# Performance work log

Hardware: AMD Instinct MI355X
Metric: run time of the kernel (lower is better)

The kernel has to match this reference:

```python
import jax, jax.numpy as jnp
import numpy as np

U = 8          # units per modular layer
B = 16384      # batch
IN = 512       # input feature dim
H = 512        # modular hidden dim
NC = 62        # n_class


def _aggregate(P, h):
    # P: [T, F] policy link matrix; h: [F, B, D] per-unit features.
    # agg[t] = sum_f P[t,f] * h[f], normalized by row-sum when row-sum > 0.
    s = jnp.einsum('tf,fbd->tbd', P, h)
    row = P.sum(axis=1)                      # [T]
    safe = jnp.where(row > 0, row, 1.0)[:, None, None]
    return jnp.where((row > 0)[:, None, None], s / safe, s)


def setup_inputs() -> dict:
    key = jax.random.key(0)
    ks = jax.random.split(key, 12)
    s_in = 1.0 / np.sqrt(IN)
    s_h = 1.0 / np.sqrt(H)
    return {
        'x': jax.random.normal(ks[0], (B, IN), jnp.float32),
        'policy1': jax.random.uniform(ks[1], (U * U,), jnp.float32),
        'policy2': jax.random.uniform(ks[2], (U * U,), jnp.float32),
        'policy_final': jax.random.uniform(ks[3], (U,), jnp.float32),
        'W0': jax.random.uniform(ks[4], (U, IN, H), jnp.float32, -s_in, s_in),
        'b0': jax.random.uniform(ks[5], (U, H), jnp.float32, -s_in, s_in),
        'W1': jax.random.uniform(ks[6], (U, H, H), jnp.float32, -s_h, s_h),
        'b1': jax.random.uniform(ks[7], (U, H), jnp.float32, -s_h, s_h),
        'W2': jax.random.uniform(ks[8], (U, H, NC), jnp.float32, -s_h, s_h),
        'b2': jax.random.uniform(ks[9], (U, NC), jnp.float32, -s_h, s_h),
    }


def reference(x, policy1, policy2, policy_final, W0, b0, W1, b1, W2, b2):
    # Layer 0 (input modular layer): policy_list[0] is forced to all-ones,
    # so every unit sees x unscaled. Each unit: Linear + ReLU.
    h0 = jax.nn.relu(jnp.einsum('bi,uid->ubd', x, W0) + b0[:, None, :])  # [U,B,H]

    # Mid layer: policy-gated weighted-sum aggregation, then per-unit Linear+ReLU.
    a1 = _aggregate(policy1.reshape(U, U), h0)
    h1 = jax.nn.relu(jnp.einsum('ubi,uid->ubd', a1, W1) + b1[:, None, :])

    # Output modular layer: aggregate then per-unit Linear (no activation).
    a2 = _aggregate(policy2.reshape(U, U), h1)
    h2 = jnp.einsum('ubi,uic->ubc', a2, W2) + b2[:, None, :]  # [U,B,NC]

    # Final gating. Original code divides by divider INSIDE the unit loop
    # (every iteration), so replicate that recurrence exactly.
    d = policy_final.sum()
    inv = jnp.where(d > 0, 1.0 / jnp.where(d > 0, d, 1.0), 1.0)
    out = jnp.zeros((B, NC), jnp.float32)
    for j in range(U):  # fixed small unit count, not a data dim
        out = (out + h2[j] * policy_final[j]) * inv
    return out
```

## Files before the change

kernel.cpp:

```cpp
#include <hip/hip_runtime.h>

#define U_   8
#define B_   16384
#define NC_  62

typedef __attribute__((ext_vector_type(8))) short bfrag;
typedef __attribute__((ext_vector_type(4))) float facc;

__device__ __forceinline__ float bf2f(unsigned int lo16) {
    union { unsigned int i; float f; } v;
    v.i = lo16 << 16;
    return v.f;
}
__device__ __forceinline__ unsigned short f2bf(float f) {
    unsigned int x = __float_as_uint(f);
    return (unsigned short)((x + 0x7fffu + ((x >> 16) & 1u)) >> 16);
}
__device__ __forceinline__ void gl2lds16(const void* g, void* l) {
    __builtin_amdgcn_global_load_lds(
        (const __attribute__((address_space(1))) void*)g,
        (__attribute__((address_space(3))) void*)l, 16, 0, 0);
}

__global__ void prep_kernel(const float* __restrict__ p1, const float* __restrict__ p2,
                            const float* __restrict__ pf, const float* __restrict__ b2,
                            float* __restrict__ P1n, float* __restrict__ P2n,
                            float* __restrict__ wfin, float* __restrict__ cconst)
{
    int t = threadIdx.x;
    if (t >= 64) return;
    int row = t >> 3;
    float s1 = 0.f, s2 = 0.f;
    for (int f = 0; f < 8; f++) { s1 += p1[row * 8 + f]; s2 += p2[row * 8 + f]; }
    P1n[t] = p1[t] * (s1 > 0.f ? 1.f / s1 : 1.f);
    P2n[t] = p2[t] * (s2 > 0.f ? 1.f / s2 : 1.f);
    float d = 0.f;
    for (int j = 0; j < 8; j++) d += pf[j];
    float inv = d > 0.f ? 1.f / d : 1.f;
    float wv[8];
    for (int j = 0; j < 8; j++) {
        float v = pf[j];
        for (int i = j; i < 8; i++) v *= inv;
        wv[j] = v;
    }
    if (t < 8) wfin[t] = wv[t];
    float cc = 0.f;
    if (t < NC_) for (int u = 0; u < 8; u++) cc += wv[u] * b2[u * NC_ + t];
    cconst[t] = cc;
}

__global__ __launch_bounds__(256) void reorder_w0(
    const float* __restrict__ W0, unsigned short* __restrict__ W0r)
{
    __shared__ float tile[32][33];
    const int u  = blockIdx.z;
    const int n0 = blockIdx.x * 32, k0 = blockIdx.y * 32;
    const int tx = threadIdx.x & 31, ty = threadIdx.x >> 5;
    const float* Wb = W0 + (long)u * 512 * 512;
#pragma unroll
    for (int i = 0; i < 4; i++)
        tile[ty + i * 8][tx] = Wb[(long)(k0 + ty + i * 8) * 512 + n0 + tx];
    __syncthreads();
#pragma unroll
    for (int i = 0; i < 4; i++) {
        int n = n0 + ty + i * 8, k = k0 + tx;
        int np = (n >> 5) * 256 + u * 32 + (n & 31);
        W0r[(long)np * 512 + k] = f2bf(tile[tx][ty + i * 8]);
    }
}

__global__ __launch_bounds__(256) void transpose_w(
    const float* __restrict__ W, unsigned short* __restrict__ Wt)
{
    __shared__ float tile[32][33];
    const int u  = blockIdx.z;
    const int n0 = blockIdx.x * 32, k0 = blockIdx.y * 32;
    const int tx = threadIdx.x & 31, ty = threadIdx.x >> 5;
    const float* Wb = W + (long)u * 512 * 512;
#pragma unroll
    for (int i = 0; i < 4; i++)
        tile[ty + i * 8][tx] = Wb[(long)(k0 + ty + i * 8) * 512 + n0 + tx];
    __syncthreads();
    unsigned short* Wo = Wt + (long)u * 512 * 512;
#pragma unroll
    for (int i = 0; i < 4; i++) {
        int n = n0 + ty + i * 8, k = k0 + tx;
        Wo[(long)n * 512 + k] = f2bf(tile[tx][ty + i * 8]);
    }
}

__global__ __launch_bounds__(256) void wout_build(
    const float* __restrict__ W2, const float* __restrict__ P2n,
    const float* __restrict__ wfin, unsigned short* __restrict__ Woutt)
{
    const int c   = threadIdx.x & 63;
    const int row = blockIdx.x * 4 + (threadIdx.x >> 6);
    const int f = row >> 9, k = row & 511;
    float s = 0.f;
    if (c < NC_) {
#pragma unroll
        for (int u = 0; u < 8; u++)
            s += wfin[u] * P2n[u * 8 + f] * W2[((long)u * 512 + k) * NC_ + c];
    }
    Woutt[(long)c * 4096 + row] = f2bf(s);
}

__global__ __launch_bounds__(256) void convert_x(
    const float* __restrict__ x, unsigned short* __restrict__ xb, long n)
{
    long i = ((long)blockIdx.x * 256 + threadIdx.x) * 8;
    if (i >= n) return;
    const float4* xp = (const float4*)(x + i);
    float4 a = xp[0], b = xp[1];
    uint4 o;
    o.x = f2bf(a.x) | ((unsigned)f2bf(a.y) << 16);
    o.y = f2bf(a.z) | ((unsigned)f2bf(a.w) << 16);
    o.z = f2bf(b.x) | ((unsigned)f2bf(b.y) << 16);
    o.w = f2bf(b.z) | ((unsigned)f2bf(b.w) << 16);
    *(uint4*)(xb + i) = o;
}

__global__ __launch_bounds__(512, 4) void gemm0_mix(
    const unsigned short* __restrict__ xb, const unsigned short* __restrict__ W0r,
    const float* __restrict__ b0, const float* __restrict__ P1n,
    unsigned short* __restrict__ a1, long plane)
{
    __shared__ __align__(16) unsigned short sm[128 * 264];
    unsigned short* sA = sm;
    unsigned short* sB = sm + 128 * 64;
    const int tid = threadIdx.x, w = tid >> 6, lane = tid & 63;
    const int flat = blockIdx.x;
    const int xcd = flat & 7, seq = flat >> 3;
    const int ng = xcd * 2 + (seq & 1);
    const long mBase = (long)(seq >> 1) * 128;

    const int lr = lane >> 3;
    const int lg = (lane & 7) ^ lr;
    const int wm = w >> 2, wn = w & 3;
    const int r = lane & 15, q = lane >> 4;
    const int x7 = r & 7;

    facc acc[4][4];
#pragma unroll
    for (int i = 0; i < 4; i++)
#pragma unroll
        for (int j = 0; j < 4; j++) acc[i][j] = (facc){0.f, 0.f, 0.f, 0.f};

    for (int k0 = 0; k0 < 512; k0 += 64) {
        __syncthreads();
#pragma unroll
        for (int i = 0; i < 2; i++) {
            const int c = w + i * 8;
            gl2lds16(xb + (mBase + c * 8 + lr) * 512 + k0 + lg * 8, sA + c * 512);
        }
#pragma unroll
        for (int i = 0; i < 4; i++) {
            const int c = w * 4 + i;
            gl2lds16(W0r + ((long)ng * 256 + c * 8 + lr) * 512 + k0 + lg * 8,
                     sB + c * 512);
        }
        __syncthreads();
#pragma unroll
        for (int h = 0; h < 2; h++) {
            const int xg = ((h * 4 + q) ^ x7) * 8;
            bfrag aF[4], bF[4];
#pragma unroll
            for (int mt = 0; mt < 4; mt++)
                aF[mt] = *(const bfrag*)&sA[(wm * 64 + mt * 16 + r) * 64 + xg];
#pragma unroll
            for (int nt = 0; nt < 4; nt++)
                bF[nt] = *(const bfrag*)&sB[(wn * 64 + nt * 16 + r) * 64 + xg];
#pragma unroll
            for (int mt = 0; mt < 4; mt++)
#pragma unroll
                for (int nt = 0; nt < 4; nt++)
                    acc[mt][nt] = __builtin_amdgcn_mfma_f32_16x16x32_bf16(
                        aF[mt], bF[nt], acc[mt][nt], 0, 0, 0);
        }
    }

    __syncthreads();
#pragma unroll
    for (int nt = 0; nt < 4; nt++) {
        const int cl = wn * 64 + nt * 16 + r;
        const float bv = b0[(cl >> 5) * 512 + ng * 32 + (cl & 31)];
#pragma unroll
        for (int mt = 0; mt < 4; mt++) {
            const int rowb = wm * 64 + mt * 16 + q * 4;
#pragma unroll
            for (int rg = 0; rg < 4; rg++) {
                float v = acc[mt][nt][rg] + bv;
                v = v > 0.f ? v : 0.f;
                sm[(rowb + rg) * 264 + cl] = f2bf(v);
            }
        }
    }
    __syncthreads();

    float pw[64];
#pragma unroll
    for (int i = 0; i < 64; i++) pw[i] = P1n[i];
    const int row = tid >> 2, fs = (tid & 3) * 8;
    float hv[8][8];
#pragma unroll
    for (int u = 0; u < 8; u++) {
        bfrag hx = *(const bfrag*)&sm[row * 264 + u * 32 + fs];
#pragma unroll
        for (int j = 0; j < 8; j++)
            hv[u][j] = bf2f((unsigned int)(unsigned short)hx[j]);
    }
    const long rowOff = (mBase + row) * 512 + ng * 32 + fs;
#pragma unroll
    for (int t = 0; t < 8; t++) {
        float o[8];
#pragma unroll
        for (int j = 0; j < 8; j++) {
            float s = 0.f;
#pragma unroll
            for (int u = 0; u < 8; u++) s = fmaf(pw[t * 8 + u], hv[u][j], s);
            o[j] = s;
        }
        uint4 ov;
        ov.x = f2bf(o[0]) | ((unsigned)f2bf(o[1]) << 16);
        ov.y = f2bf(o[2]) | ((unsigned)f2bf(o[3]) << 16);
        ov.z = f2bf(o[4]) | ((unsigned)f2bf(o[5]) << 16);
        ov.w = f2bf(o[6]) | ((unsigned)f2bf(o[7]) << 16);
        *(uint4*)(a1 + (long)t * plane + rowOff) = ov;
    }
}

__global__ __launch_bounds__(256, 4) void gemm_h(
    const unsigned short* __restrict__ a1,
    const unsigned short* __restrict__ W1t,
    const float* __restrict__ b1,
    unsigned short* __restrict__ h1, long plane)
{
    __shared__ __align__(16) unsigned short sm[128 * 136];
    unsigned short* sA = sm;
    unsigned short* sB = sm + 128 * 64;
    const int tid = threadIdx.x, w = tid >> 6, lane = tid & 63;
    const int flat = blockIdx.x;
    const int u = flat & 7, seq = flat >> 3;
    const int nBase = (seq & 3) * 128;
    const long mBase = (long)(seq >> 2) * 128;

    const int lr = lane >> 3, lg = (lane & 7) ^ lr;
    const int wm = w >> 1, wn = w & 1;
    const int r = lane & 15, q = lane >> 4;
    const int x7 = r & 7;

    const unsigned short* Ab = a1 + (long)u * plane;
    const unsigned short* Bb = W1t + ((long)u * 512 + nBase) * 512;

    facc acc[4][4];
#pragma unroll
    for (int i = 0; i < 4; i++)
#pragma unroll
        for (int j = 0; j < 4; j++) acc[i][j] = (facc){0.f, 0.f, 0.f, 0.f};

    for (int k0 = 0; k0 < 512; k0 += 64) {
        __syncthreads();
#pragma unroll
        for (int i = 0; i < 4; i++) {
            const int c = w * 4 + i;
            gl2lds16(Ab + (mBase + c * 8 + lr) * 512 + k0 + lg * 8, sA + c * 512);
            gl2lds16(Bb + (long)(c * 8 + lr) * 512 + k0 + lg * 8, sB + c * 512);
        }
        __syncthreads();
#pragma unroll
        for (int h = 0; h < 2; h++) {
            const int xg = ((h * 4 + q) ^ x7) * 8;
            bfrag aF[4], bF[4];
#pragma unroll
            for (int mt = 0; mt < 4; mt++)
                aF[mt] = *(const bfrag*)&sA[(wm * 64 + mt * 16 + r) * 64 + xg];
#pragma unroll
            for (int nt = 0; nt < 4; nt++)
                bF[nt] = *(const bfrag*)&sB[(wn * 64 + nt * 16 + r) * 64 + xg];
#pragma unroll
            for (int mt = 0; mt < 4; mt++)
#pragma unroll
                for (int nt = 0; nt < 4; nt++)
                    acc[mt][nt] = __builtin_amdgcn_mfma_f32_16x16x32_bf16(
                        aF[mt], bF[nt], acc[mt][nt], 0, 0, 0);
        }
    }

    __syncthreads();
#pragma unroll
    for (int nt = 0; nt < 4; nt++) {
        const int col = wn * 64 + nt * 16 + r;
        const float bv = b1[u * 512 + nBase + col];
#pragma unroll
        for (int mt = 0; mt < 4; mt++) {
            const int rowb = wm * 64 + mt * 16 + q * 4;
#pragma unroll
            for (int rg = 0; rg < 4; rg++) {
                float v = acc[mt][nt][rg] + bv;
                v = v > 0.f ? v : 0.f;
                sm[(rowb + rg) * 136 + col] = f2bf(v);
            }
        }
    }
    __syncthreads();

    unsigned short* Cb = h1 + (long)u * plane + mBase * 512 + nBase;
#pragma unroll
    for (int it = 0; it < 8; it++) {
        const int g = tid + it * 256;
        const int row = g >> 4, gr = g & 15;
        *(uint4*)(Cb + (long)row * 512 + gr * 8) = *(const uint4*)&sm[row * 136 + gr * 8];
    }
}

__global__ __launch_bounds__(256, 4) void gemm_out(
    const unsigned short* __restrict__ h1,
    const unsigned short* __restrict__ Bt,
    float* __restrict__ partial, long plane, int Bc)
{
    __shared__ __align__(16) unsigned short sA[64 * 64];
    __shared__ __align__(16) unsigned short sB[64 * 64];
    const int tid = threadIdx.x, w = tid >> 6, lane = tid & 63;
    const int flat = blockIdx.x;
    const int kc = flat & 1;
    const long mBase = (long)(flat >> 1) * 64;

    const int lr = lane >> 3, lg = (lane & 7) ^ lr;
    const int wm = w >> 1, wn = w & 1;
    const int r = lane & 15, q = lane >> 4;
    const int x7 = r & 7;

    facc acc[2][2];
#pragma unroll
    for (int i = 0; i < 2; i++)
#pragma unroll
        for (int j = 0; j < 2; j++) acc[i][j] = (facc){0.f, 0.f, 0.f, 0.f};

    for (int it = 0; it < 32; it++) {
        const int u = kc * 4 + (it >> 3);
        const int kk = (it & 7) * 64;
        __syncthreads();
#pragma unroll
        for (int i = 0; i < 2; i++) {
            const int c = w * 2 + i;
            gl2lds16(h1 + (long)u * plane + (mBase + c * 8 + lr) * 512 + kk + lg * 8,
                     sA + c * 512);
            gl2lds16(Bt + (long)(c * 8 + lr) * 4096 + u * 512 + kk + lg * 8,
                     sB + c * 512);
        }
        __syncthreads();
#pragma unroll
        for (int h = 0; h < 2; h++) {
            const int xg = ((h * 4 + q) ^ x7) * 8;
            bfrag aF[2], bF[2];
#pragma unroll
            for (int mt = 0; mt < 2; mt++)
                aF[mt] = *(const bfrag*)&sA[(wm * 32 + mt * 16 + r) * 64 + xg];
#pragma unroll
            for (int nt = 0; nt < 2; nt++)
                bF[nt] = *(const bfrag*)&sB[(wn * 32 + nt * 16 + r) * 64 + xg];
#pragma unroll
            for (int mt = 0; mt < 2; mt++)
#pragma unroll
                for (int nt = 0; nt < 2; nt++)
                    acc[mt][nt] = __builtin_amdgcn_mfma_f32_16x16x32_bf16(
                        aF[mt], bF[nt], acc[mt][nt], 0, 0, 0);
        }
    }

    float* pb = partial + ((long)kc * Bc + mBase) * 64;
#pragma unroll
    for (int nt = 0; nt < 2; nt++) {
        const int col = wn * 32 + nt * 16 + r;
#pragma unroll
        for (int mt = 0; mt < 2; mt++) {
#pragma unroll
            for (int rg = 0; rg < 4; rg++) {
                const int row = wm * 32 + mt * 16 + q * 4 + rg;
                pb[(long)row * 64 + col] = acc[mt][nt][rg];
            }
        }
    }
}

__global__ __launch_bounds__(256) void reduce_out(
    const float* __restrict__ partial, const float* __restrict__ cconst,
    float* __restrict__ out, int Bc)
{
    const long flat = (long)blockIdx.x * 256 + threadIdx.x;
    const long row = flat >> 2;
    const int cg = (int)(flat & 3) * 16;
    float s[16];
#pragma unroll
    for (int j = 0; j < 16; j++) s[j] = 0.f;
#pragma unroll
    for (int kc = 0; kc < 2; kc++) {
        const float4* p = (const float4*)(partial + ((long)kc * Bc + row) * 64 + cg);
#pragma unroll
        for (int v4 = 0; v4 < 4; v4++) {
            float4 v = p[v4];
            s[v4 * 4 + 0] += v.x; s[v4 * 4 + 1] += v.y;
            s[v4 * 4 + 2] += v.z; s[v4 * 4 + 3] += v.w;
        }
    }
#pragma unroll
    for (int j = 0; j < 16; j++) {
        const int c = cg + j;
        if (c < NC_) out[row * NC_ + c] = s[j] + cconst[c];
    }
}

extern "C" void kernel_launch(void* const* d_in, const int* in_sizes, int n_in,
                              void* d_out, int out_size, void* d_ws, size_t ws_size,
                              hipStream_t stream)
{
    const float* x  = (const float*)d_in[0];
    const float* p1 = (const float*)d_in[1];
    const float* p2 = (const float*)d_in[2];
    const float* pf = (const float*)d_in[3];
    const float* W0 = (const float*)d_in[4];
    const float* b0 = (const float*)d_in[5];
    const float* W1 = (const float*)d_in[6];
    const float* b1 = (const float*)d_in[7];
    const float* W2 = (const float*)d_in[8];
    const float* b2 = (const float*)d_in[9];
    float* out = (float*)d_out;

    char* ws = (char*)d_ws;
    size_t off = 0;
    auto alloc = [&](size_t bytes) -> void* {
        void* p = ws + off;
        off += (bytes + 255) & ~(size_t)255;
        return p;
    };
    float* P1n    = (float*)alloc(64 * sizeof(float));
    float* P2n    = (float*)alloc(64 * sizeof(float));
    float* wfin   = (float*)alloc(8 * sizeof(float));
    float* cconst = (float*)alloc(64 * sizeof(float));
    unsigned short* W0r   = (unsigned short*)alloc((size_t)4096 * 512 * 2);
    unsigned short* W1t   = (unsigned short*)alloc((size_t)U_ * 512 * 512 * 2);
    unsigned short* Woutt = (unsigned short*)alloc((size_t)64 * 4096 * 2);
    unsigned short* xb    = (unsigned short*)alloc((size_t)B_ * 512 * 2);

    size_t remain = ws_size > off ? ws_size - off : 0;
    int Bc = 2048;
    for (int cand = B_; cand >= 2048; cand >>= 1) {
        size_t need = 2ull * 8 * cand * 512 * 2 + 2ull * cand * 64 * 4 + 1024;
        if (need <= remain) { Bc = cand; break; }
    }
    unsigned short* a1 = (unsigned short*)alloc(8ull * Bc * 512 * 2);
    unsigned short* h1 = (unsigned short*)alloc(8ull * Bc * 512 * 2);
    float* partial     = (float*)alloc(2ull * Bc * 64 * 4);

    prep_kernel<<<1, 64, 0, stream>>>(p1, p2, pf, b2, P1n, P2n, wfin, cconst);
    reorder_w0<<<dim3(16, 16, 8), 256, 0, stream>>>(W0, W0r);
    transpose_w<<<dim3(16, 16, 8), 256, 0, stream>>>(W1, W1t);
    wout_build<<<dim3(1024), 256, 0, stream>>>(W2, P2n, wfin, Woutt);
    convert_x<<<dim3(B_ * 512 / 8 / 256), 256, 0, stream>>>(x, xb, (long)B_ * 512);

    const int Mb = Bc / 128;
    const long plane = (long)Bc * 512;
    for (int bb = 0; bb < B_; bb += Bc) {
        gemm0_mix<<<dim3(16 * Mb), 512, 0, stream>>>(
            xb + (long)bb * 512, W0r, b0, P1n, a1, plane);
        gemm_h<<<dim3(32 * Mb), 256, 0, stream>>>(a1, W1t, b1, h1, plane);
        gemm_out<<<dim3(2 * (Bc / 64)), 256, 0, stream>>>(h1, Woutt, partial, plane, Bc);
        reduce_out<<<dim3(Bc / 64), 256, 0, stream>>>(
            partial, cconst, out + (long)bb * NC_, Bc);
    }
}
```

Before: 327.1 us.

## Fuse hidden-layer GEMM with output GEMM to avoid h1 round trip

Merges gemm_h and gemm_out into one kernel. Each block computes a 64-row tile of h1 for two units, one 128-column slab at a time, and stages that slab in LDS as bf16. It then multiplies the slab straight into the output accumulator using Woutt fragments loaded from global memory. This drops the h1 workspace write and read and one launch, at the cost of smaller M tiles (less reuse of W1), more synchronisation, unstaged global loads of B fragments for the second GEMM, and a 4-way partial reduction instead of 2-way.

```diff
diff --git a/kernel.cpp b/kernel.cpp
--- a/kernel.cpp
+++ b/kernel.cpp
@@ -229,146 +229,126 @@
     }
 }
 
-__global__ __launch_bounds__(256, 4) void gemm_h(
+__global__ __launch_bounds__(256, 4) void gemm_h_out(
     const unsigned short* __restrict__ a1,
     const unsigned short* __restrict__ W1t,
     const float* __restrict__ b1,
-    unsigned short* __restrict__ h1, long plane)
-{
-    __shared__ __align__(16) unsigned short sm[128 * 136];
-    unsigned short* sA = sm;
-    unsigned short* sB = sm + 128 * 64;
+    const unsigned short* __restrict__ Woutt,
+    float* __restrict__ partial, long plane, int Bc)
+{
+    __shared__ __align__(16) unsigned short sA[64 * 64];
+    __shared__ __align__(16) unsigned short sB[128 * 64];
+    __shared__ __align__(16) unsigned short sH[2 * 64 * 64];
     const int tid = threadIdx.x, w = tid >> 6, lane = tid & 63;
     const int flat = blockIdx.x;
-    const int u = flat & 7, seq = flat >> 3;
-    const int nBase = (seq & 3) * 128;
-    const long mBase = (long)(seq >> 2) * 128;
+    const int xcd = flat & 7, seq = flat >> 3;
+    const int up = xcd >> 1;
+    const int Mt2 = Bc >> 7;
+    const long mBase = ((long)(xcd & 1) * Mt2 + seq) * 64;
 
     const int lr = lane >> 3, lg = (lane & 7) ^ lr;
     const int wm = w >> 1, wn = w & 1;
     const int r = lane & 15, q = lane >> 4;
     const int x7 = r & 7;
 
-    const unsigned short* Ab = a1 + (long)u * plane;
-    const unsigned short* Bb = W1t + ((long)u * 512 + nBase) * 512;
-
-    facc acc[4][4];
-#pragma unroll
-    for (int i = 0; i < 4; i++)
-#pragma unroll
-        for (int j = 0; j < 4; j++) acc[i][j] = (facc){0.f, 0.f, 0.f, 0.f};
-
-    for (int k0 = 0; k0 < 512; k0 += 64) {
-        __syncthreads();
-#pragma unroll
-        for (int i = 0; i < 4; i++) {
-            const int c = w * 4 + i;
-            gl2lds16(Ab + (mBase + c * 8 + lr) * 512 + k0 + lg * 8, sA + c * 512);
-            gl2lds16(Bb + (long)(c * 8 + lr) * 512 + k0 + lg * 8, sB + c * 512);
-        }
-        __syncthreads();
-#pragma unroll
-        for (int h = 0; h < 2; h++) {
-            const int xg = ((h * 4 + q) ^ x7) * 8;
-            bfrag aF[4], bF[4];
-#pragma unroll
-            for (int mt = 0; mt < 4; mt++)
-                aF[mt] = *(const bfrag*)&sA[(wm * 64 + mt * 16 + r) * 64 + xg];
-#pragma unroll
-            for (int nt = 0; nt < 4; nt++)
-                bF[nt] = *(const bfrag*)&sB[(wn * 64 + nt * 16 + r) * 64 + xg];
-#pragma unroll
-            for (int mt = 0; mt < 4; mt++)
-#pragma unroll
-                for (int nt = 0; nt < 4; nt++)
-                    acc[mt][nt] = __builtin_amdgcn_mfma_f32_16x16x32_bf16(
-                        aF[mt], bF[nt], acc[mt][nt], 0, 0, 0);
-        }
-    }
-
-    __syncthreads();
-#pragma unroll
-    for (int nt = 0; nt < 4; nt++) {
-        const int col = wn * 64 + nt * 16 + r;
-        const float bv = b1[u * 512 + nBase + col];
-#pragma unroll
-        for (int mt = 0; mt < 4; mt++) {
-            const int rowb = wm * 64 + mt * 16 + q * 4;
-#pragma unroll
-            for (int rg = 0; rg < 4; rg++) {
-                float v = acc[mt][nt][rg] + bv;
-                v = v > 0.f ? v : 0.f;
-                sm[(rowb + rg) * 136 + col] = f2bf(v);
+    facc acc2[2][2];
+#pragma unroll
+    for (int i = 0; i < 2; i++)
+#pragma unroll
+        for (int j = 0; j < 2; j++) acc2[i][j] = (facc){0.f, 0.f, 0.f, 0.f};
+
+    for (int iu = 0; iu < 2; iu++) {
+        const int u = up * 2 + iu;
+        const unsigned short* Ab = a1 + (long)u * plane;
+        for (int nb = 0; nb < 4; nb++) {
+            const int nBase = nb * 128;
+            facc acc1[2][4];
+#pragma unroll
+            for (int i = 0; i < 2; i++)
+#pragma unroll
+                for (int j = 0; j < 4; j++) acc1[i][j] = (facc){0.f, 0.f, 0.f, 0.f};
+
+            for (int k0 = 0; k0 < 512; k0 += 64) {
+                __syncthreads();
+#pragma unroll
+                for (int i = 0; i < 2; i++) {
+                    const int c = w * 2 + i;
+                    gl2lds16(Ab + (mBase + c * 8 + lr) * 512 + k0 + lg * 8,
+                             sA + c * 512);
+                }
+#pragma unroll
+                for (int i = 0; i < 4; i++) {
+                    const int c = w * 4 + i;
+                    gl2lds16(W1t + ((long)u * 512 + nBase + c * 8 + lr) * 512
+                                 + k0 + lg * 8, sB + c * 512);
+                }
+                __syncthreads();
+#pragma unroll
+                for (int h = 0; h < 2; h++) {
+                    const int xg = ((h * 4 + q) ^ x7) * 8;
+                    bfrag aF[2], bF[4];
+#pragma unroll
+                    for (int mt = 0; mt < 2; mt++)
+                        aF[mt] = *(const bfrag*)&sA[(wm * 32 + mt * 16 + r) * 64 + xg];
+#pragma unroll
+                    for (int nt = 0; nt < 4; nt++)
+                        bF[nt] = *(const bfrag*)&sB[(wn * 64 + nt * 16 + r) * 64 + xg];
+#pragma unroll
+                    for (int mt = 0; mt < 2; mt++)
+#pragma unroll
+                        for (int nt = 0; nt < 4; nt++)
+                            acc1[mt][nt] = __builtin_amdgcn_mfma_f32_16x16x32_bf16(
+                                aF[mt], bF[nt], acc1[mt][nt], 0, 0, 0);
+                }
             }
-        }
-    }
-    __syncthreads();
-
-    unsigned short* Cb = h1 + (long)u * plane + mBase * 512 + nBase;
-#pragma unroll
-    for (int it = 0; it < 8; it++) {
-        const int g = tid + it * 256;
-        const int row = g >> 4, gr = g & 15;
-        *(uint4*)(Cb + (long)row * 512 + gr * 8) = *(const uint4*)&sm[row * 136 + gr * 8];
-    }
-}
-
-__global__ __launch_bounds__(256, 4) void gemm_out(
-    const unsigned short* __restrict__ h1,
-    const unsigned short* __restrict__ Bt,
-    float* __restrict__ partial, long plane, int Bc)
-{
-    __shared__ __align__(16) unsigned short sA[64 * 64];
-    __shared__ __align__(16) unsigned short sB[64 * 64];
-    const int tid = threadIdx.x, w = tid >> 6, lane = tid & 63;
-    const int flat = blockIdx.x;
-    const int kc = flat & 1;
-    const long mBase = (long)(flat >> 1) * 64;
-
-    const int lr = lane >> 3, lg = (lane & 7) ^ lr;
-    const int wm = w >> 1, wn = w & 1;
-    const int r = lane & 15, q = lane >> 4;
-    const int x7 = r & 7;
-
-    facc acc[2][2];
-#pragma unroll
-    for (int i = 0; i < 2; i++)
-#pragma unroll
-        for (int j = 0; j < 2; j++) acc[i][j] = (facc){0.f, 0.f, 0.f, 0.f};
-
-    for (int it = 0; it < 32; it++) {
-        const int u = kc * 4 + (it >> 3);
-        const int kk = (it & 7) * 64;
-        __syncthreads();
-#pragma unroll
-        for (int i = 0; i < 2; i++) {
-            const int c = w * 2 + i;
-            gl2lds16(h1 + (long)u * plane + (mBase + c * 8 + lr) * 512 + kk + lg * 8,
-                     sA + c * 512);
-            gl2lds16(Bt + (long)(c * 8 + lr) * 4096 + u * 512 + kk + lg * 8,
-                     sB + c * 512);
-        }
-        __syncthreads();
-#pragma unroll
-        for (int h = 0; h < 2; h++) {
-            const int xg = ((h * 4 + q) ^ x7) * 8;
-            bfrag aF[2], bF[2];
-#pragma unroll
-            for (int mt = 0; mt < 2; mt++)
-                aF[mt] = *(const bfrag*)&sA[(wm * 32 + mt * 16 + r) * 64 + xg];
-#pragma unroll
-            for (int nt = 0; nt < 2; nt++)
-                bF[nt] = *(const bfrag*)&sB[(wn * 32 + nt * 16 + r) * 64 + xg];
-#pragma unroll
-            for (int mt = 0; mt < 2; mt++)
-#pragma unroll
-                for (int nt = 0; nt < 2; nt++)
-                    acc[mt][nt] = __builtin_amdgcn_mfma_f32_16x16x32_bf16(
-                        aF[mt], bF[nt], acc[mt][nt], 0, 0, 0);
-        }
-    }
-
-    float* pb = partial + ((long)kc * Bc + mBase) * 64;
+
+#pragma unroll
+            for (int nt = 0; nt < 4; nt++) {
+                const int col = wn * 64 + nt * 16 + r;
+                const float bv = b1[u * 512 + nBase + col];
+                const int slab = col >> 6, cg = (col >> 3) & 7, ce = col & 7;
+#pragma unroll
+                for (int mt = 0; mt < 2; mt++) {
+                    const int rowb = wm * 32 + mt * 16 + q * 4;
+#pragma unroll
+                    for (int rg = 0; rg < 4; rg++) {
+                        const int row = rowb + rg;
+                        float v = acc1[mt][nt][rg] + bv;
+                        v = v > 0.f ? v : 0.f;
+                        sH[slab * 4096 + row * 64 + ((cg ^ (row & 7)) * 8) + ce] = f2bf(v);
+                    }
+                }
+            }
+            __syncthreads();
+
+#pragma unroll
+            for (int ks = 0; ks < 4; ks++) {
+                const int kh = ks >> 1, h2 = ks & 1;
+                bfrag aF2[2], bF2[2];
+#pragma unroll
+                for (int mt = 0; mt < 2; mt++) {
+                    const int row = wm * 32 + mt * 16 + r;
+                    aF2[mt] = *(const bfrag*)&sH[kh * 4096 + row * 64
+                                                 + (((h2 * 4 + q) ^ x7) * 8)];
+                }
+#pragma unroll
+                for (int nt = 0; nt < 2; nt++) {
+                    const int c = wn * 32 + nt * 16 + r;
+                    bF2[nt] = *(const bfrag*)(Woutt + (long)c * 4096 + u * 512
+                                              + nBase + ks * 32 + q * 8);
+                }
+#pragma unroll
+                for (int mt = 0; mt < 2; mt++)
+#pragma unroll
+                    for (int nt = 0; nt < 2; nt++)
+                        acc2[mt][nt] = __builtin_amdgcn_mfma_f32_16x16x32_bf16(
+                            aF2[mt], bF2[nt], acc2[mt][nt], 0, 0, 0);
+            }
+            __syncthreads();
+        }
+    }
+
+    float* pb = partial + ((long)up * Bc + mBase) * 64;
 #pragma unroll
     for (int nt = 0; nt < 2; nt++) {
         const int col = wn * 32 + nt * 16 + r;
@@ -377,7 +357,7 @@
 #pragma unroll
             for (int rg = 0; rg < 4; rg++) {
                 const int row = wm * 32 + mt * 16 + q * 4 + rg;
-                pb[(long)row * 64 + col] = acc[mt][nt][rg];
+                pb[(long)row * 64 + col] = acc2[mt][nt][rg];
             }
         }
     }
@@ -394,8 +374,8 @@
 #pragma unroll
     for (int j = 0; j < 16; j++) s[j] = 0.f;
 #pragma unroll
-    for (int kc = 0; kc < 2; kc++) {
-        const float4* p = (const float4*)(partial + ((long)kc * Bc + row) * 64 + cg);
+    for (int up = 0; up < 4; up++) {
+        const float4* p = (const float4*)(partial + ((long)up * Bc + row) * 64 + cg);
 #pragma unroll
         for (int v4 = 0; v4 < 4; v4++) {
             float4 v = p[v4];
@@ -445,12 +425,11 @@
     size_t remain = ws_size > off ? ws_size - off : 0;
     int Bc = 2048;
     for (int cand = B_; cand >= 2048; cand >>= 1) {
-        size_t need = 2ull * 8 * cand * 512 * 2 + 2ull * cand * 64 * 4 + 1024;
+        size_t need = 8ull * cand * 512 * 2 + 4ull * cand * 64 * 4 + 1024;
         if (need <= remain) { Bc = cand; break; }
     }
     unsigned short* a1 = (unsigned short*)alloc(8ull * Bc * 512 * 2);
-    unsigned short* h1 = (unsigned short*)alloc(8ull * Bc * 512 * 2);
-    float* partial     = (float*)alloc(2ull * Bc * 64 * 4);
+    float* partial     = (float*)alloc(4ull * Bc * 64 * 4);
 
     prep_kernel<<<1, 64, 0, stream>>>(p1, p2, pf, b2, P1n, P2n, wfin, cconst);
     reorder_w0<<<dim3(16, 16, 8), 256, 0, stream>>>(W0, W0r);
@@ -463,8 +442,8 @@
     for (int bb = 0; bb < B_; bb += Bc) {
         gemm0_mix<<<dim3(16 * Mb), 512, 0, stream>>>(
             xb + (long)bb * 512, W0r, b0, P1n, a1, plane);
-        gemm_h<<<dim3(32 * Mb), 256, 0, stream>>>(a1, W1t, b1, h1, plane);
-        gemm_out<<<dim3(2 * (Bc / 64)), 256, 0, stream>>>(h1, Woutt, partial, plane, Bc);
+        gemm_h_out<<<dim3(Bc / 16), 256, 0, stream>>>(
+            a1, W1t, b1, Woutt, partial, plane, Bc);
         reduce_out<<<dim3(Bc / 64), 256, 0, stream>>>(
             partial, cconst, out + (long)bb * NC_, Bc);
     }
```

New measurement: 390.0 us. 1.19x slower.
